# Optimization experiments

Hardware: AMD Instinct MI355X
Metric: run time of the kernel (lower is better)

Reference implementation:

```python
import math
import jax, jax.numpy as jnp
import numpy as np

B = 32768
D = 64
LR = 0.01
ADAM_EPS = 1e-8
LN_EPS = 1e-5


def _pe0(d):
    # positional encoding at position 0: sin(0)=0 on even dims, cos(0)=1 on odd dims
    div = jnp.exp(jnp.arange(0, d, 2, dtype=jnp.float32) * (-math.log(10000.0) / d))
    pe = jnp.zeros((d,), jnp.float32)
    pe = pe.at[0::2].set(jnp.sin(0.0 * div))
    pe = pe.at[1::2].set(jnp.cos(0.0 * div))
    return pe


def setup_inputs() -> dict:
    key = jax.random.key(0)
    ks = jax.random.split(key, 32)
    n = lambda i, shape, s=1.0: jax.random.normal(ks[i], shape, jnp.float32) * s
    inp = {
        'input1': n(0, (B, 500, 3)),
        'input2': n(1, (B, 250, 3)),
        'input3': n(2, (B, 50, 3)),
        'input4': n(3, (B, 1, 3)),
        # conv weights [out_ch, in_ch, K]
        'w_l': n(4, (3, 3, 500), 0.02), 'b_l': n(5, (3,), 0.02),
        'w_m': n(6, (3, 3, 250), 0.03), 'b_m': n(7, (3,), 0.02),
        'w_s': n(8, (3, 3, 50), 0.08), 'b_s': n(9, (3,), 0.02),
        'fc1_w': n(10, (D, 12), 0.2), 'fc1_b': n(11, (D,), 0.02),
        'q_w': n(12, (D, D), 0.1), 'q_b': n(13, (D,), 0.02),
        'k_w': n(14, (D, D), 0.1), 'k_b': n(15, (D,), 0.02),
        'v_w': n(16, (D, D), 0.1), 'v_b': n(17, (D,), 0.02),
        # Task params (torch.randn -> std 1, but scaled down for numeric sanity)
        't_k': n(18, (D, D), 0.1), 't_v': n(19, (D, D), 0.1), 't_q': n(20, (D, D), 0.1),
        # Learner inner linear
        'lw': n(21, (D, D), 0.1), 'lb': n(22, (D,), 0.02),
        'ln_g': jnp.ones((D,), jnp.float32), 'ln_b': jnp.zeros((D,), jnp.float32),
        'out_w': n(23, (1, D), 0.1), 'out_b': n(24, (1,), 0.02),
    }
    return inp


def reference(input1, input2, input3, input4, w_l, b_l, w_m, b_m, w_s, b_s,
              fc1_w, fc1_b, q_w, q_b, k_w, k_b, v_w, v_b,
              t_k, t_v, t_q, lw, lb, ln_g, ln_b, out_w, out_b):
    # convs have kernel == seq length -> output length 1 -> full-window contraction
    x_l = jnp.einsum('bkc,ock->bo', input1, w_l) + b_l  # [B,3]
    x_m = jnp.einsum('bkc,ock->bo', input2, w_m) + b_m
    x_s = jnp.einsum('bkc,ock->bo', input3, w_s) + b_s
    cat = jnp.concatenate([x_l, x_m, x_s, input4[:, 0, :]], axis=-1)  # [B,12]
    h = cat @ fc1_w.T + fc1_b + _pe0(D)  # [B,64], seq dim is 1 (implicit)

    q = h @ q_w.T + q_b
    k = h @ k_w.T + k_b
    v = h @ v_w.T + v_b
    s = jnp.concatenate([q, k, v], axis=0)  # [3B,64] (dropout is identity in eval)

    # --- TTLinear: one inner Adam step (fresh optimizer state -> step 1) ---
    tv = s @ t_k          # train view
    lv = s @ t_v          # label view
    pred = tv @ lw.T + lb
    g = (2.0 / pred.size) * (pred - lv)   # d(MSE)/d(pred)
    gW = g.T @ tv                          # [64,64] grad wrt lw
    gb = g.sum(0)
    # Adam step 1: m_hat = g, v_hat = g^2 -> update = lr * g / (|g| + eps)
    lw1 = lw - LR * gW / (jnp.sqrt(gW * gW) + ADAM_EPS)
    lb1 = lb - LR * gb / (jnp.sqrt(gb * gb) + ADAM_EPS)
    o = (s @ t_q) @ lw1.T + lb1           # predict

    # LayerNorm + SiLU
    mu = o.mean(-1, keepdims=True)
    var = ((o - mu) ** 2).mean(-1, keepdims=True)
    normed = (o - mu) / jnp.sqrt(var + LN_EPS) * ln_g + ln_b
    a = normed * jax.nn.sigmoid(normed)

    last = a[a.shape[0] * 2 // 3:]        # last third -> [B,64]
    return last @ out_w.T + out_b          # [B,1]
```

## Files before the change

kernel.cpp:

```cpp
#include <hip/hip_runtime.h>
#include <cstdint>


__global__ void k_prep(const float* __restrict__ wl, const float* __restrict__ wm,
                       const float* __restrict__ wsx, float* __restrict__ wt) {
  int tid = blockIdx.x * 256 + threadIdx.x;
  if (tid < 4500) {
    int o = tid / 1500, e = tid % 1500, k = e / 3, c = e % 3;
    wt[tid] = wl[o * 1500 + c * 500 + k];
  } else if (tid < 6750) {
    int r = tid - 4500; int o = r / 750, e = r % 750, k = e / 3, c = e % 3;
    wt[tid] = wm[o * 750 + c * 250 + k];
  } else if (tid < 7200) {
    int r = tid - 6750; int o = r / 150, e = r % 150, k = e / 3, c = e % 3;
    wt[tid] = wsx[o * 150 + c * 50 + k];
  }
}

__global__ void __launch_bounds__(256) k_front(
    const float* __restrict__ in1, const float* __restrict__ in2,
    const float* __restrict__ in3, const float* __restrict__ in4,
    const float* __restrict__ bl, const float* __restrict__ bm,
    const float* __restrict__ bs_,
    const float* __restrict__ fc1w, const float* __restrict__ fc1b,
    const float* __restrict__ wt, float* __restrict__ hout)
{
  __shared__ __align__(16) float wsh[7200];
  {
    const float4* s4 = (const float4*)wt;
    float4* d4 = (float4*)wsh;
    for (int i = threadIdx.x; i < 1800; i += 256) d4[i] = s4[i];
  }

  const int l   = threadIdx.x & 63;
  const int w   = threadIdx.x >> 6;
  const int sub = l >> 4;
  const int t   = l & 15;
  const int b0  = blockIdx.x * 16 + w * 4;
  const size_t b = (size_t)(b0 + sub);

  float fw[12];
  #pragma unroll
  for (int i = 0; i < 12; ++i) fw[i] = fc1w[l * 12 + i];
  float hb = fc1b[l] + ((l & 1) ? 1.0f : 0.0f);
  hb += bl[0]*fw[0] + bl[1]*fw[1] + bl[2]*fw[2]
      + bm[0]*fw[3] + bm[1]*fw[4] + bm[2]*fw[5]
      + bs_[0]*fw[6] + bs_[1]*fw[7] + bs_[2]*fw[8];

  __syncthreads();

  float a0=0,a1=0,a2=0,a3=0,a4=0,a5=0,a6=0,a7=0,a8=0;

  {
    const float4* r  = (const float4*)(in1 + b * 1500);
    const float4* u0 = (const float4*)(wsh);
    const float4* u1 = (const float4*)(wsh + 1500);
    const float4* u2 = (const float4*)(wsh + 3000);
    #pragma unroll
    for (int c = 0; c < 2; ++c) {
      float4 vb[8];
      #pragma unroll
      for (int j = 0; j < 8; ++j) vb[j] = r[t + 16*(c*8 + j)];
      #pragma unroll
      for (int j = 0; j < 8; ++j) {
        const int g = t + 16*(c*8 + j);
        float4 v = vb[j], w0 = u0[g], w1 = u1[g], w2 = u2[g];
        a0 += v.x*w0.x + v.y*w0.y + v.z*w0.z + v.w*w0.w;
        a1 += v.x*w1.x + v.y*w1.y + v.z*w1.z + v.w*w1.w;
        a2 += v.x*w2.x + v.y*w2.y + v.z*w2.z + v.w*w2.w;
      }
    }
    {
      float4 vb[7];
      #pragma unroll
      for (int j = 0; j < 7; ++j) vb[j] = r[t + 16*(16 + j)];
      #pragma unroll
      for (int j = 0; j < 7; ++j) {
        const int g = t + 16*(16 + j);
        float4 v = vb[j], w0 = u0[g], w1 = u1[g], w2 = u2[g];
        a0 += v.x*w0.x + v.y*w0.y + v.z*w0.z + v.w*w0.w;
        a1 += v.x*w1.x + v.y*w1.y + v.z*w1.z + v.w*w1.w;
        a2 += v.x*w2.x + v.y*w2.y + v.z*w2.z + v.w*w2.w;
      }
    }
    if (t < 7) {
      const int g = 368 + t;
      float4 v = r[g], w0 = u0[g], w1 = u1[g], w2 = u2[g];
      a0 += v.x*w0.x + v.y*w0.y + v.z*w0.z + v.w*w0.w;
      a1 += v.x*w1.x + v.y*w1.y + v.z*w1.z + v.w*w1.w;
      a2 += v.x*w2.x + v.y*w2.y + v.z*w2.z + v.w*w2.w;
    }
  }

  {
    const float2* r  = (const float2*)(in2 + b * 750);
    const float2* u0 = (const float2*)(wsh + 4500);
    const float2* u1 = (const float2*)(wsh + 5250);
    const float2* u2 = (const float2*)(wsh + 6000);
    #pragma unroll
    for (int c = 0; c < 2; ++c) {
      float2 vb[8];
      #pragma unroll
      for (int j = 0; j < 8; ++j) vb[j] = r[t + 16*(c*8 + j)];
      #pragma unroll
      for (int j = 0; j < 8; ++j) {
        const int g = t + 16*(c*8 + j);
        float2 v = vb[j], w0 = u0[g], w1 = u1[g], w2 = u2[g];
        a3 += v.x*w0.x + v.y*w0.y;
        a4 += v.x*w1.x + v.y*w1.y;
        a5 += v.x*w2.x + v.y*w2.y;
      }
    }
    {
      float2 vb[7];
      #pragma unroll
      for (int j = 0; j < 7; ++j) vb[j] = r[t + 16*(16 + j)];
      #pragma unroll
      for (int j = 0; j < 7; ++j) {
        const int g = t + 16*(16 + j);
        float2 v = vb[j], w0 = u0[g], w1 = u1[g], w2 = u2[g];
        a3 += v.x*w0.x + v.y*w0.y;
        a4 += v.x*w1.x + v.y*w1.y;
        a5 += v.x*w2.x + v.y*w2.y;
      }
    }
    if (t < 7) {
      const int g = 368 + t;
      float2 v = r[g], w0 = u0[g], w1 = u1[g], w2 = u2[g];
      a3 += v.x*w0.x + v.y*w0.y;
      a4 += v.x*w1.x + v.y*w1.y;
      a5 += v.x*w2.x + v.y*w2.y;
    }
  }

  {
    const float2* r  = (const float2*)(in3 + b * 150);
    const float2* u0 = (const float2*)(wsh + 6750);
    const float2* u1 = (const float2*)(wsh + 6900);
    const float2* u2 = (const float2*)(wsh + 7050);
    {
      float2 vb[4];
      #pragma unroll
      for (int j = 0; j < 4; ++j) vb[j] = r[t + 16*j];
      #pragma unroll
      for (int j = 0; j < 4; ++j) {
        const int g = t + 16*j;
        float2 v = vb[j], w0 = u0[g], w1 = u1[g], w2 = u2[g];
        a6 += v.x*w0.x + v.y*w0.y;
        a7 += v.x*w1.x + v.y*w1.y;
        a8 += v.x*w2.x + v.y*w2.y;
      }
    }
    if (t < 11) {
      const int g = 64 + t;
      float2 v = r[g], w0 = u0[g], w1 = u1[g], w2 = u2[g];
      a6 += v.x*w0.x + v.y*w0.y;
      a7 += v.x*w1.x + v.y*w1.y;
      a8 += v.x*w2.x + v.y*w2.y;
    }
  }

  #pragma unroll
  for (int m = 1; m <= 8; m <<= 1) {
    a0 += __shfl_xor(a0, m, 64); a1 += __shfl_xor(a1, m, 64);
    a2 += __shfl_xor(a2, m, 64); a3 += __shfl_xor(a3, m, 64);
    a4 += __shfl_xor(a4, m, 64); a5 += __shfl_xor(a5, m, 64);
    a6 += __shfl_xor(a6, m, 64); a7 += __shfl_xor(a7, m, 64);
    a8 += __shfl_xor(a8, m, 64);
  }
  #pragma unroll
  for (int q = 0; q < 4; ++q) {
    float c0 = __shfl(a0, q*16, 64), c1 = __shfl(a1, q*16, 64), c2 = __shfl(a2, q*16, 64);
    float c3 = __shfl(a3, q*16, 64), c4 = __shfl(a4, q*16, 64), c5 = __shfl(a5, q*16, 64);
    float c6 = __shfl(a6, q*16, 64), c7 = __shfl(a7, q*16, 64), c8 = __shfl(a8, q*16, 64);
    int bb = b0 + q;
    const float* p4 = in4 + (size_t)bb * 3;
    float hv = hb + c0*fw[0] + c1*fw[1] + c2*fw[2] + c3*fw[3] + c4*fw[4]
                  + c5*fw[5] + c6*fw[6] + c7*fw[7] + c8*fw[8]
                  + p4[0]*fw[9] + p4[1]*fw[10] + p4[2]*fw[11];
    hout[(size_t)bb * 64 + l] = hv;
  }
}

__global__ void __launch_bounds__(256) k_gram(const float* __restrict__ h,
                                              float* __restrict__ part) {
  __shared__ float hs[64][64];
  const int tid = threadIdx.x;
  const int r0 = (tid >> 4) << 2, c0 = (tid & 15) << 2;
  float acc[4][4] = {{0.f}};
  float sv = 0.f;
  for (int tile = 0; tile < 2; ++tile) {
    __syncthreads();
    const size_t trow = (size_t)(blockIdx.x * 2 + tile) * 64;
    const float4* src = (const float4*)(h + trow * 64);
    #pragma unroll
    for (int i = 0; i < 4; ++i) ((float4*)hs)[tid + 256*i] = src[tid + 256*i];
    __syncthreads();
    for (int k = 0; k < 64; ++k) {
      float4 av = *(const float4*)&hs[k][r0];
      float4 bv = *(const float4*)&hs[k][c0];
      float ar[4] = {av.x,av.y,av.z,av.w}, br[4] = {bv.x,bv.y,bv.z,bv.w};
      #pragma unroll
      for (int i = 0; i < 4; ++i)
        #pragma unroll
        for (int j = 0; j < 4; ++j) acc[i][j] += ar[i]*br[j];
    }
    if (tid < 64) { for (int k = 0; k < 64; ++k) sv += hs[k][tid]; }
  }
  float* dst = part + (size_t)blockIdx.x * 4160;
  #pragma unroll
  for (int i = 0; i < 4; ++i)
    *(float4*)&dst[(r0+i)*64 + c0] = make_float4(acc[i][0], acc[i][1], acc[i][2], acc[i][3]);
  if (tid < 64) dst[4096 + tid] = sv;
}

__global__ void k_gred(const float* __restrict__ part, float* __restrict__ out) {
  int e = blockIdx.x * 256 + threadIdx.x;
  if (e >= 4160) return;
  float s = 0.f;
  for (int p = 0; p < 256; ++p) s += part[(size_t)p * 4160 + e];
  out[e] = s;
}

#define MM_TILE(DST, SA, SB, OPEQ)                                             \
  for (int k = 0; k < 64; ++k) {                                               \
    float4 av = *(const float4*)&SA[k][r0];                                    \
    float4 bv = *(const float4*)&SB[k][c0];                                    \
    float ar_[4] = {av.x,av.y,av.z,av.w};                                      \
    float br_[4] = {bv.x,bv.y,bv.z,bv.w};                                      \
    _Pragma("unroll") for (int i_ = 0; i_ < 4; ++i_)                           \
    _Pragma("unroll") for (int j_ = 0; j_ < 4; ++j_)                           \
      DST[i_][j_] OPEQ ar_[i_]*br_[j_];                                        \
  }
#define STAGE_N(DSTBUF, SRC) for (int i = threadIdx.x; i < 1024; i += 256) {   \
    int r_ = i >> 4, c_ = (i & 15) << 2;                                       \
    *(float4*)&DSTBUF[r_][c_] = ((const float4*)(SRC))[i]; }
#define STAGE_T(DSTBUF, SRC) for (int i = threadIdx.x; i < 4096; i += 256) {   \
    int r_ = i >> 6, k_ = i & 63; DSTBUF[k_][r_] = (SRC)[i]; }

__global__ void __launch_bounds__(256) k_small(
    const float* __restrict__ h2hs,
    const float* __restrict__ qw, const float* __restrict__ qb_,
    const float* __restrict__ kw, const float* __restrict__ kb_,
    const float* __restrict__ vw, const float* __restrict__ vb_,
    const float* __restrict__ tk, const float* __restrict__ tv_,
    const float* __restrict__ tq, const float* __restrict__ lw,
    const float* __restrict__ lb_, float* __restrict__ wobo)
{
  __shared__ float BA[64][68];
  __shared__ float BB[64][68];
  __shared__ float BC[64][68];
  __shared__ float sm[512];
  const int tid = threadIdx.x;
  const int r0 = (tid >> 4) << 2;
  const int c0 = (tid & 15) << 2;

  STAGE_N(BC, h2hs);
  if (tid < 64) sm[tid] = h2hs[4096 + tid];
  __syncthreads();

  float s2[4][4] = {{0.f}};
  {
    const float* Wp_[3] = {qw, kw, vw};
    for (int p = 0; p < 3; ++p) {
      __syncthreads();
      STAGE_T(BA, Wp_[p]);
      __syncthreads();
      if (tid < 64) {
        float s = 0.f;
        for (int k = 0; k < 64; ++k) s += BA[k][tid] * sm[k];
        sm[64*(1+p) + tid] = s;
      }
      float g4[4][4] = {{0.f}};
      MM_TILE(g4, BA, BC, +=);
      #pragma unroll
      for (int i = 0; i < 4; ++i)
        #pragma unroll
        for (int j = 0; j < 4; ++j) BB[c0+j][r0+i] = g4[i][j];
      __syncthreads();
      MM_TILE(s2, BB, BA, +=);
    }
  }
  __syncthreads();
  if (tid < 64) {
    float ss = sm[64+tid] + sm[128+tid] + sm[192+tid]
             + 32768.f * (qb_[tid] + kb_[tid] + vb_[tid]);
    sm[256 + tid] = ss;
  }
  {
    const float* bp_[3] = {qb_, kb_, vb_};
    #pragma unroll
    for (int p = 0; p < 3; ++p) {
      float ar[4], ac[4], br[4], bc4[4];
      #pragma unroll
      for (int i = 0; i < 4; ++i) { ar[i] = sm[64*(1+p)+r0+i]; br[i] = bp_[p][r0+i]; }
      #pragma unroll
      for (int j = 0; j < 4; ++j) { ac[j] = sm[64*(1+p)+c0+j]; bc4[j] = bp_[p][c0+j]; }
      #pragma unroll
      for (int i = 0; i < 4; ++i)
        #pragma unroll
        for (int j = 0; j < 4; ++j)
          s2[i][j] += ar[i]*bc4[j] + br[i]*ac[j] + 32768.f*br[i]*bc4[j];
    }
  }
  #pragma unroll
  for (int i = 0; i < 4; ++i)
    #pragma unroll
    for (int j = 0; j < 4; ++j) BA[r0+i][c0+j] = s2[i][j];
  STAGE_N(BC, tk);
  __syncthreads();
  if (tid < 64) {
    float s = 0.f;
    for (int k = 0; k < 64; ++k) s += BC[k][tid] * sm[256+k];
    sm[320 + tid] = s;
  }
  float y4[4][4] = {{0.f}};
  MM_TILE(y4, BA, BC, +=);
  __syncthreads();
  #pragma unroll
  for (int i = 0; i < 4; ++i)
    #pragma unroll
    for (int j = 0; j < 4; ++j) BB[r0+i][c0+j] = y4[i][j];
  STAGE_N(BA, tv_);
  __syncthreads();
  if (tid < 64) {
    float s = 0.f;
    for (int k = 0; k < 64; ++k) s += BA[k][tid] * sm[256+k];
    sm[448 + tid] = s;
  }
  float core[4][4] = {{0.f}}, z4[4][4] = {{0.f}};
  for (int k = 0; k < 64; ++k) {
    float4 av1 = *(const float4*)&BA[k][r0];
    float4 av2 = *(const float4*)&BC[k][r0];
    float4 bv  = *(const float4*)&BB[k][c0];
    float a1_[4] = {av1.x,av1.y,av1.z,av1.w};
    float a2_[4] = {av2.x,av2.y,av2.z,av2.w};
    float b_[4]  = {bv.x,bv.y,bv.z,bv.w};
    #pragma unroll
    for (int i = 0; i < 4; ++i)
      #pragma unroll
      for (int j = 0; j < 4; ++j) { core[i][j] -= a1_[i]*b_[j]; z4[i][j] += a2_[i]*b_[j]; }
  }
  __syncthreads();
  #pragma unroll
  for (int i = 0; i < 4; ++i)
    #pragma unroll
    for (int j = 0; j < 4; ++j) BA[r0+i][c0+j] = z4[i][j];
  STAGE_T(BC, lw);
  __syncthreads();
  MM_TILE(core, BC, BA, +=);
  const float cg = 2.0f / 6291456.0f;
  float l1t[4][4];
  #pragma unroll
  for (int i = 0; i < 4; ++i) {
    float lbi = lb_[r0+i];
    #pragma unroll
    for (int j = 0; j < 4; ++j) {
      float gw  = cg * (core[i][j] + lbi * sm[320 + c0 + j]);
      float lwv = lw[(r0+i)*64 + (c0+j)];
      l1t[i][j] = lwv - 0.01f * gw / (fabsf(gw) + 1e-8f);
    }
  }
  __syncthreads();
  #pragma unroll
  for (int i = 0; i < 4; ++i)
    #pragma unroll
    for (int j = 0; j < 4; ++j) BB[c0+j][r0+i] = l1t[i][j];
  if (tid < 64) {
    float s = 0.f;
    for (int c = 0; c < 64; ++c) s += lw[tid*64 + c] * sm[320 + c];
    float gb = cg * (s - sm[448 + tid] + 98304.f * lb_[tid]);
    sm[384 + tid] = lb_[tid] - 0.01f * gb / (fabsf(gb) + 1e-8f);
  }
  STAGE_T(BC, tq);
  __syncthreads();
  float u4[4][4] = {{0.f}};
  MM_TILE(u4, BC, BB, +=);
  __syncthreads();
  #pragma unroll
  for (int i = 0; i < 4; ++i)
    #pragma unroll
    for (int j = 0; j < 4; ++j) BA[r0+i][c0+j] = u4[i][j];
  STAGE_N(BC, vw);
  __syncthreads();
  float w4[4][4] = {{0.f}};
  MM_TILE(w4, BC, BA, +=);
  #pragma unroll
  for (int i = 0; i < 4; ++i)
    *(float4*)&wobo[(r0+i)*64 + c0] = make_float4(w4[i][0], w4[i][1], w4[i][2], w4[i][3]);
  if (tid < 64) {
    float s = 0.f;
    for (int a = 0; a < 64; ++a) s += vb_[a] * BA[a][tid];
    wobo[4096 + tid] = s + sm[384 + tid];
  }
}

__global__ void __launch_bounds__(256) k_out(
    const float* __restrict__ h, const float* __restrict__ wobo,
    const float* __restrict__ lng, const float* __restrict__ lnb,
    const float* __restrict__ outw, const float* __restrict__ outb,
    float* __restrict__ out)
{
  const size_t b = (size_t)blockIdx.x * 256 + threadIdx.x;
  const float* hr = h + b * 64;
  float o[64];
  #pragma unroll
  for (int j = 0; j < 64; ++j) o[j] = wobo[4096 + j];
  #pragma unroll 1
  for (int i = 0; i < 64; i += 4) {
    float4 hv = *(const float4*)(hr + i);
    const float* wr0 = wobo + (i+0)*64;
    const float* wr1 = wobo + (i+1)*64;
    const float* wr2 = wobo + (i+2)*64;
    const float* wr3 = wobo + (i+3)*64;
    #pragma unroll
    for (int j = 0; j < 64; ++j) o[j] += hv.x * wr0[j];
    #pragma unroll
    for (int j = 0; j < 64; ++j) o[j] += hv.y * wr1[j];
    #pragma unroll
    for (int j = 0; j < 64; ++j) o[j] += hv.z * wr2[j];
    #pragma unroll
    for (int j = 0; j < 64; ++j) o[j] += hv.w * wr3[j];
  }
  float mu = 0.f;
  #pragma unroll
  for (int j = 0; j < 64; ++j) mu += o[j];
  mu *= (1.0f/64.0f);
  float var = 0.f;
  #pragma unroll
  for (int j = 0; j < 64; ++j) { float d = o[j] - mu; var += d*d; }
  var *= (1.0f/64.0f);
  float inv = rsqrtf(var + 1e-5f);
  float accv = outb[0];
  #pragma unroll
  for (int j = 0; j < 64; ++j) {
    float n = (o[j] - mu) * inv * lng[j] + lnb[j];
    float a = n / (1.0f + __expf(-n));
    accv += a * outw[j];
  }
  out[b] = accv;
}

extern "C" void kernel_launch(void* const* d_in, const int* in_sizes, int n_in,
                              void* d_out, int out_size, void* d_ws, size_t ws_size,
                              hipStream_t stream) {
  const float* in1  = (const float*)d_in[0];
  const float* in2  = (const float*)d_in[1];
  const float* in3  = (const float*)d_in[2];
  const float* in4  = (const float*)d_in[3];
  const float* w_l  = (const float*)d_in[4];
  const float* b_l  = (const float*)d_in[5];
  const float* w_m  = (const float*)d_in[6];
  const float* b_m  = (const float*)d_in[7];
  const float* w_s  = (const float*)d_in[8];
  const float* b_s  = (const float*)d_in[9];
  const float* fc1w = (const float*)d_in[10];
  const float* fc1b = (const float*)d_in[11];
  const float* q_w  = (const float*)d_in[12];
  const float* q_b  = (const float*)d_in[13];
  const float* k_w  = (const float*)d_in[14];
  const float* k_b  = (const float*)d_in[15];
  const float* v_w  = (const float*)d_in[16];
  const float* v_b  = (const float*)d_in[17];
  const float* t_k  = (const float*)d_in[18];
  const float* t_v  = (const float*)d_in[19];
  const float* t_q  = (const float*)d_in[20];
  const float* lw   = (const float*)d_in[21];
  const float* lb   = (const float*)d_in[22];
  const float* ln_g = (const float*)d_in[23];
  const float* ln_b = (const float*)d_in[24];
  const float* outw = (const float*)d_in[25];
  const float* outb = (const float*)d_in[26];

  float* ws   = (float*)d_ws;
  float* WT   = ws;
  float* H    = ws + 7200;
  float* PART = H + 2097152;
  float* H2   = PART + 1064960;
  float* WOBO = H2 + 4160;

  k_prep <<<29,   256, 0, stream>>>(w_l, w_m, w_s, WT);
  k_front<<<2048, 256, 0, stream>>>(in1, in2, in3, in4, b_l, b_m, b_s,
                                    fc1w, fc1b, WT, H);
  k_gram <<<256,  256, 0, stream>>>(H, PART);
  k_gred <<<17,   256, 0, stream>>>(PART, H2);
  k_small<<<1,    256, 0, stream>>>(H2, q_w, q_b, k_w, k_b, v_w, v_b,
                                    t_k, t_v, t_q, lw, lb, WOBO);
  k_out  <<<128,  256, 0, stream>>>(H, WOBO, ln_g, ln_b, outw, outb,
                                    (float*)d_out);
}
```

Baseline: 157.5 us.

## Parallelize Gram reduction, QKV Gram stage, and output kernel across more blocks

The 256-way partial Gram reduction becomes two stages (136 blocks reducing 32 partials each, then 17 blocks finishing). The single-block QKV Gram computation is split across 3 blocks, one per projection, and their results are summed in the next kernel. The output kernel moves from 128 blocks of 256 threads to 256 blocks of 128 threads so more CUs are busy. The aim is to cut the serial tail work, at the cost of two extra kernel launches and some extra workspace traffic.

After: 142.7 us. 1.1x faster.

```diff
diff --git a/kernel.cpp b/kernel.cpp
--- a/kernel.cpp
+++ b/kernel.cpp
@@ -214,12 +214,24 @@
   if (tid < 64) dst[4096 + tid] = sv;
 }
 
-__global__ void k_gred(const float* __restrict__ part, float* __restrict__ out) {
-  int e = blockIdx.x * 256 + threadIdx.x;
+__global__ void k_gred1(const float* __restrict__ part, float* __restrict__ part2) {
+  const int g = blockIdx.x % 17;
+  const int s = blockIdx.x / 17;
+  const int e = g * 256 + threadIdx.x;
   if (e >= 4160) return;
-  float s = 0.f;
-  for (int p = 0; p < 256; ++p) s += part[(size_t)p * 4160 + e];
-  out[e] = s;
+  float sum = 0.f;
+  const float* p0 = part + (size_t)(s * 32) * 4160 + e;
+  #pragma unroll 8
+  for (int p = 0; p < 32; ++p) sum += p0[(size_t)p * 4160];
+  part2[(size_t)s * 4160 + e] = sum;
+}
+__global__ void k_gred2(const float* __restrict__ part2, float* __restrict__ out) {
+  const int e = blockIdx.x * 256 + threadIdx.x;
+  if (e >= 4160) return;
+  float sum = 0.f;
+  #pragma unroll
+  for (int s = 0; s < 8; ++s) sum += part2[(size_t)s * 4160 + e];
+  out[e] = sum;
 }
 
 #define MM_TILE(DST, SA, SB, OPEQ)                                             \
@@ -238,14 +250,69 @@
 #define STAGE_T(DSTBUF, SRC) for (int i = threadIdx.x; i < 4096; i += 256) {   \
     int r_ = i >> 6, k_ = i & 63; DSTBUF[k_][r_] = (SRC)[i]; }
 
-__global__ void __launch_bounds__(256) k_small(
+__global__ void __launch_bounds__(256) k_small1(
     const float* __restrict__ h2hs,
     const float* __restrict__ qw, const float* __restrict__ qb_,
     const float* __restrict__ kw, const float* __restrict__ kb_,
     const float* __restrict__ vw, const float* __restrict__ vb_,
+    float* __restrict__ s2p)
+{
+  __shared__ float BA[64][68];
+  __shared__ float BB[64][68];
+  __shared__ float BC[64][68];
+  __shared__ float sm[128];
+  const int tid = threadIdx.x;
+  const int r0 = (tid >> 4) << 2;
+  const int c0 = (tid & 15) << 2;
+  const int p  = blockIdx.x;
+  const float* Wp = (p == 0) ? qw : (p == 1) ? kw : vw;
+  const float* bp = (p == 0) ? qb_ : (p == 1) ? kb_ : vb_;
+
+  STAGE_N(BC, h2hs);
+  if (tid < 64) sm[tid] = h2hs[4096 + tid];
+  STAGE_T(BA, Wp);
+  __syncthreads();
+  if (tid < 64) {
+    float s = 0.f;
+    for (int k = 0; k < 64; ++k) s += BA[k][tid] * sm[k];
+    sm[64 + tid] = s;
+    s2p[(size_t)p * 4160 + 4096 + tid] = s;
+  }
+  float g4[4][4] = {{0.f}};
+  MM_TILE(g4, BA, BC, +=);
+  #pragma unroll
+  for (int i = 0; i < 4; ++i)
+    #pragma unroll
+    for (int j = 0; j < 4; ++j) BB[c0+j][r0+i] = g4[i][j];
+  __syncthreads();
+  float s2[4][4] = {{0.f}};
+  MM_TILE(s2, BB, BA, +=);
+  {
+    float ar[4], ac[4], br[4], bc4[4];
+    #pragma unroll
+    for (int i = 0; i < 4; ++i) { ar[i] = sm[64+r0+i]; br[i] = bp[r0+i]; }
+    #pragma unroll
+    for (int j = 0; j < 4; ++j) { ac[j] = sm[64+c0+j]; bc4[j] = bp[c0+j]; }
+    #pragma unroll
+    for (int i = 0; i < 4; ++i)
+      #pragma unroll
+      for (int j = 0; j < 4; ++j)
+        s2[i][j] += ar[i]*bc4[j] + br[i]*ac[j] + 32768.f*br[i]*bc4[j];
+  }
+  #pragma unroll
+  for (int i = 0; i < 4; ++i)
+    *(float4*)&s2p[(size_t)p * 4160 + (r0+i)*64 + c0] =
+        make_float4(s2[i][0], s2[i][1], s2[i][2], s2[i][3]);
+}
+
+__global__ void __launch_bounds__(256) k_small2(
+    const float* __restrict__ s2p,
+    const float* __restrict__ qb_, const float* __restrict__ kb_,
+    const float* __restrict__ vb_,
     const float* __restrict__ tk, const float* __restrict__ tv_,
     const float* __restrict__ tq, const float* __restrict__ lw,
-    const float* __restrict__ lb_, float* __restrict__ wobo)
+    const float* __restrict__ lb_, const float* __restrict__ vw,
+    float* __restrict__ wobo)
 {
   __shared__ float BA[64][68];
   __shared__ float BB[64][68];
@@ -255,59 +322,20 @@
   const int r0 = (tid >> 4) << 2;
   const int c0 = (tid & 15) << 2;
 
-  STAGE_N(BC, h2hs);
-  if (tid < 64) sm[tid] = h2hs[4096 + tid];
-  __syncthreads();
-
-  float s2[4][4] = {{0.f}};
-  {
-    const float* Wp_[3] = {qw, kw, vw};
-    for (int p = 0; p < 3; ++p) {
-      __syncthreads();
-      STAGE_T(BA, Wp_[p]);
-      __syncthreads();
-      if (tid < 64) {
-        float s = 0.f;
-        for (int k = 0; k < 64; ++k) s += BA[k][tid] * sm[k];
-        sm[64*(1+p) + tid] = s;
-      }
-      float g4[4][4] = {{0.f}};
-      MM_TILE(g4, BA, BC, +=);
-      #pragma unroll
-      for (int i = 0; i < 4; ++i)
-        #pragma unroll
-        for (int j = 0; j < 4; ++j) BB[c0+j][r0+i] = g4[i][j];
-      __syncthreads();
-      MM_TILE(s2, BB, BA, +=);
-    }
-  }
-  __syncthreads();
+  for (int i = tid; i < 1024; i += 256) {
+    int r_ = i >> 4, c_ = (i & 15) << 2;
+    float4 v0 = ((const float4*)(s2p))[i];
+    float4 v1 = ((const float4*)(s2p + 4160))[i];
+    float4 v2 = ((const float4*)(s2p + 8320))[i];
+    *(float4*)&BA[r_][c_] = make_float4(v0.x+v1.x+v2.x, v0.y+v1.y+v2.y,
+                                        v0.z+v1.z+v2.z, v0.w+v1.w+v2.w);
+  }
+  STAGE_N(BC, tk);
   if (tid < 64) {
-    float ss = sm[64+tid] + sm[128+tid] + sm[192+tid]
+    float ss = s2p[4096 + tid] + s2p[4160 + 4096 + tid] + s2p[8320 + 4096 + tid]
              + 32768.f * (qb_[tid] + kb_[tid] + vb_[tid]);
     sm[256 + tid] = ss;
   }
-  {
-    const float* bp_[3] = {qb_, kb_, vb_};
-    #pragma unroll
-    for (int p = 0; p < 3; ++p) {
-      float ar[4], ac[4], br[4], bc4[4];
-      #pragma unroll
-      for (int i = 0; i < 4; ++i) { ar[i] = sm[64*(1+p)+r0+i]; br[i] = bp_[p][r0+i]; }
-      #pragma unroll
-      for (int j = 0; j < 4; ++j) { ac[j] = sm[64*(1+p)+c0+j]; bc4[j] = bp_[p][c0+j]; }
-      #pragma unroll
-      for (int i = 0; i < 4; ++i)
-        #pragma unroll
-        for (int j = 0; j < 4; ++j)
-          s2[i][j] += ar[i]*bc4[j] + br[i]*ac[j] + 32768.f*br[i]*bc4[j];
-    }
-  }
-  #pragma unroll
-  for (int i = 0; i < 4; ++i)
-    #pragma unroll
-    for (int j = 0; j < 4; ++j) BA[r0+i][c0+j] = s2[i][j];
-  STAGE_N(BC, tk);
   __syncthreads();
   if (tid < 64) {
     float s = 0.f;
@@ -395,13 +423,13 @@
   }
 }
 
-__global__ void __launch_bounds__(256) k_out(
+__global__ void __launch_bounds__(128) k_out(
     const float* __restrict__ h, const float* __restrict__ wobo,
     const float* __restrict__ lng, const float* __restrict__ lnb,
     const float* __restrict__ outw, const float* __restrict__ outb,
     float* __restrict__ out)
 {
-  const size_t b = (size_t)blockIdx.x * 256 + threadIdx.x;
+  const size_t b = (size_t)blockIdx.x * 128 + threadIdx.x;
   const float* hr = h + b * 64;
   float o[64];
   #pragma unroll
@@ -472,20 +500,24 @@
   const float* outw = (const float*)d_in[25];
   const float* outb = (const float*)d_in[26];
 
-  float* ws   = (float*)d_ws;
-  float* WT   = ws;
-  float* H    = ws + 7200;
-  float* PART = H + 2097152;
-  float* H2   = PART + 1064960;
-  float* WOBO = H2 + 4160;
-
-  k_prep <<<29,   256, 0, stream>>>(w_l, w_m, w_s, WT);
-  k_front<<<2048, 256, 0, stream>>>(in1, in2, in3, in4, b_l, b_m, b_s,
-                                    fc1w, fc1b, WT, H);
-  k_gram <<<256,  256, 0, stream>>>(H, PART);
-  k_gred <<<17,   256, 0, stream>>>(PART, H2);
-  k_small<<<1,    256, 0, stream>>>(H2, q_w, q_b, k_w, k_b, v_w, v_b,
-                                    t_k, t_v, t_q, lw, lb, WOBO);
-  k_out  <<<128,  256, 0, stream>>>(H, WOBO, ln_g, ln_b, outw, outb,
-                                    (float*)d_out);
-}
+  float* ws    = (float*)d_ws;
+  float* WT    = ws;
+  float* H     = ws + 7200;
+  float* PART  = H + 2097152;
+  float* H2    = PART + 1064960;
+  float* WOBO  = H2 + 4160;
+  float* PART2 = WOBO + 4160;
+  float* S2P   = PART2 + 33280;
+
+  k_prep  <<<29,   256, 0, stream>>>(w_l, w_m, w_s, WT);
+  k_front <<<2048, 256, 0, stream>>>(in1, in2, in3, in4, b_l, b_m, b_s,
+                                     fc1w, fc1b, WT, H);
+  k_gram  <<<256,  256, 0, stream>>>(H, PART);
+  k_gred1 <<<136,  256, 0, stream>>>(PART, PART2);
+  k_gred2 <<<17,   256, 0, stream>>>(PART2, H2);
+  k_small1<<<3,    256, 0, stream>>>(H2, q_w, q_b, k_w, k_b, v_w, v_b, S2P);
+  k_small2<<<1,    256, 0, stream>>>(S2P, q_b, k_b, v_b, t_k, t_v, t_q,
+                                     lw, lb, v_w, WOBO);
+  k_out   <<<256,  128, 0, stream>>>(H, WOBO, ln_g, ln_b, outw, outb,
+                                     (float*)d_out);
+}
```
